# Kernel optimization log

Measured on AMD Instinct MI355X. Metric: run time of the kernel, lower is better.

## Reference

```python
import jax, jax.numpy as jnp
import numpy as np

N_HEAD = 12
CTX = 2048
FUT = 16
EPS = 1e-5


def _layer_norm(x, w, b):
    m = x.mean(-1, keepdims=True)
    v = ((x - m) ** 2).mean(-1, keepdims=True)
    return (x - m) / jnp.sqrt(v + EPS) * w + b


def setup_inputs() -> dict:
    key = jax.random.key(0)
    ks = jax.random.split(key, 10)
    C = 768
    hs = C // N_HEAD
    B, T = 1, 2048
    std = 0.02
    inp = {
        "x": jax.random.normal(ks[0], (B, T, C), jnp.float32),
        "ln1_w": jnp.ones((C,), jnp.float32),
        "ln1_b": jnp.zeros((C,), jnp.float32),
        "attn_w": jax.random.normal(ks[1], (C, 3 * C), jnp.float32) * std,
        "attn_b": jnp.zeros((3 * C,), jnp.float32),
        "fk_w": jax.random.normal(ks[2], (N_HEAD, hs, CTX - 1), jnp.float32) * std,
        "fk_b": jnp.zeros((N_HEAD, 1, CTX - 1), jnp.float32),
        "fv_w": jax.random.normal(ks[3], (N_HEAD, CTX - 1, hs), jnp.float32) * std,
        "fv_b": jnp.zeros((N_HEAD, 1, hs), jnp.float32),
        "proj_w": jax.random.normal(ks[4], (C, C), jnp.float32) * std,
        "proj_b": jnp.zeros((C,), jnp.float32),
        "ln2_w": jnp.ones((C,), jnp.float32),
        "ln2_b": jnp.zeros((C,), jnp.float32),
        "ff_w1": jax.random.normal(ks[5], (C, 4 * C), jnp.float32) * std,
        "ff_b1": jnp.zeros((4 * C,), jnp.float32),
        "ff_w2": jax.random.normal(ks[6], (4 * C, C), jnp.float32) * std,
        "ff_b2": jnp.zeros((C,), jnp.float32),
    }
    return inp


def _block(x, ln1_w, ln1_b, attn_w, attn_b, fk_w, fk_b, fv_w, fv_b,
           proj_w, proj_b, ln2_w, ln2_b, ff_w1, ff_b1, ff_w2, ff_b2):
    B, T, C = x.shape
    hs = C // N_HEAD
    T_wf = min(T + FUT, CTX)          # static
    F1 = T_wf - 1
    scale = hs ** (-0.5)

    h = _layer_norm(x, ln1_w, ln1_b)
    qkv = h @ attn_w + attn_b
    q, k, v = jnp.split(qkv, 3, axis=-1)
    q = q.reshape(B, T, N_HEAD, hs).transpose(0, 2, 1, 3)  # [B,H,T,hs]
    k = k.reshape(B, T, N_HEAD, hs).transpose(0, 2, 1, 3)
    v = v.reshape(B, T, N_HEAD, hs).transpose(0, 2, 1, 3)

    attn = jnp.einsum('bhqd,bhkd->bhqk', q, k) * scale      # [B,H,T,T]

    causal = jnp.tril(jnp.ones((T, T), bool))
    causal_attn = jnp.where(causal, attn, 0.0)
    pad = min(FUT, CTX - T)
    if pad > 0:
        causal_attn = jnp.pad(causal_attn, ((0, 0), (0, 0), (0, 0), (0, pad)))

    # future scores via per-head dynamic linear on q
    fut_bad = (jnp.tril(jnp.ones((T, F1)), -1) + jnp.triu(jnp.ones((T, F1)), FUT)) != 0
    fattn = (jnp.einsum('bhtd,hdf->bhtf', q, fk_w[:, :, :F1]) + fk_b[:, :, :F1]) * scale
    fattn = jnp.where(fut_bad, 0.0, fattn)
    fattn = jnp.pad(fattn, ((0, 0), (0, 0), (0, 0), (1, 0)))  # [B,H,T,T_wf]

    full = causal_attn + fattn
    full_ok = jnp.tril(jnp.ones((T, T_wf), bool), FUT)
    full = jnp.where(full_ok, full, -jnp.inf)
    sm = jax.nn.softmax(full, axis=-1)

    sc = jnp.where(causal, sm[..., :T], 0.0)
    sf = jnp.where(fut_bad, 0.0, sm[..., 1:T_wf])

    causal_x = jnp.einsum('bhqk,bhkd->bhqd', sc, v)
    future_x = jnp.einsum('bhtf,hfd->bhtd', sf, fv_w[:, :F1, :]) + fv_b

    new_x = (causal_x + future_x).transpose(0, 2, 1, 3).reshape(B, T, C)
    new_x = new_x @ proj_w + proj_b

    x = x + new_x
    h2 = _layer_norm(x, ln2_w, ln2_b)
    ff = jax.nn.gelu(h2 @ ff_w1 + ff_b1, approximate=False) @ ff_w2 + ff_b2
    return x + ff


def reference(x, ln1_w, ln1_b, attn_w, attn_b, fk_w, fk_b, fv_w, fv_b,
              proj_w, proj_b, ln2_w, ln2_b, ff_w1, ff_b1, ff_w2, ff_b2):
    return _block(x, ln1_w, ln1_b, attn_w, attn_b, fk_w, fk_b, fv_w, fv_b,
                  proj_w, proj_b, ln2_w, ln2_b, ff_w1, ff_b1, ff_w2, ff_b2)
```

## Files before the change

kernel.cpp:

```cpp
#include <hip/hip_runtime.h>
#include <math.h>
#include <stdint.h>
#include <stddef.h>

typedef __bf16 bf16_t;
typedef __bf16 bf16x8 __attribute__((ext_vector_type(8)));
typedef __bf16 bf16x4 __attribute__((ext_vector_type(4)));
typedef float f32x4 __attribute__((ext_vector_type(4)));

#define DEV __device__ __forceinline__


DEV void gload_lds16(const void* g, void* l) {
  __builtin_amdgcn_global_load_lds((__attribute__((address_space(1))) void*)g,
                                   (__attribute__((address_space(3))) void*)l,
                                   16, 0, 0);
}

template <bool MAXOP>
DEV float blockReduce256(float v, float* sm) {
  const int lane = threadIdx.x & 63, wid = threadIdx.x >> 6;
#pragma unroll
  for (int o = 32; o > 0; o >>= 1) {
    float ov = __shfl_down(v, o);
    v = MAXOP ? fmaxf(v, ov) : (v + ov);
  }
  if (lane == 0) sm[wid] = v;
  __syncthreads();
  float r = MAXOP ? fmaxf(fmaxf(sm[0], sm[1]), fmaxf(sm[2], sm[3]))
                  : (sm[0] + sm[1] + sm[2] + sm[3]);
  __syncthreads();
  return r;
}

__global__ __launch_bounds__(256) void prep_kernel(
    const float* __restrict__ x, const float* __restrict__ ln1_w,
    const float* __restrict__ ln1_b, bf16_t* __restrict__ hbuf,
    const float* __restrict__ attn_w, bf16_t* __restrict__ attn_wT,
    const float* __restrict__ proj_w, bf16_t* __restrict__ proj_wT,
    const float* __restrict__ ff_w1, bf16_t* __restrict__ ff_w1T,
    const float* __restrict__ ff_w2, bf16_t* __restrict__ ff_w2T,
    const float* __restrict__ fk_w, bf16_t* __restrict__ fkT,
    const float* __restrict__ fv_w, bf16_t* __restrict__ fvT) {
  __shared__ float red[4];
  __shared__ float tile[32][33];
  const int tid = threadIdx.x;
  int bid = blockIdx.x;

  if (bid < 2048) {
    const float* row = x + (size_t)bid * 768;
    float v[3];
    float s = 0.f;
#pragma unroll
    for (int i = 0; i < 3; ++i) {
      v[i] = row[tid + i * 256];
      s += v[i];
    }
    s = blockReduce256<false>(s, red);
    const float mean = s * (1.f / 768.f);
    float s2 = 0.f;
#pragma unroll
    for (int i = 0; i < 3; ++i) {
      float d = v[i] - mean;
      s2 += d * d;
    }
    s2 = blockReduce256<false>(s2, red);
    const float rstd = rsqrtf(s2 * (1.f / 768.f) + 1e-5f);
#pragma unroll
    for (int i = 0; i < 3; ++i) {
      int c = tid + i * 256;
      hbuf[(size_t)bid * 768 + c] = (bf16_t)((v[i] - mean) * rstd * ln1_w[c] + ln1_b[c]);
    }
    return;
  }
  bid -= 2048;

  const float* in;
  bf16_t* outp;
  int ldin, ldout, R, C, bx, by;
  if (bid < 1728) {
    in = attn_w; outp = attn_wT; ldin = 2304; ldout = 768; R = 768; C = 2304;
    bx = bid % 72; by = bid / 72;
  } else if (bid < 2304) {
    int k = bid - 1728;
    in = proj_w; outp = proj_wT; ldin = 768; ldout = 768; R = 768; C = 768;
    bx = k % 24; by = k / 24;
  } else if (bid < 4608) {
    int k = bid - 2304;
    in = ff_w1; outp = ff_w1T; ldin = 3072; ldout = 768; R = 768; C = 3072;
    bx = k % 96; by = k / 96;
  } else if (bid < 6912) {
    int k = bid - 4608;
    in = ff_w2; outp = ff_w2T; ldin = 768; ldout = 3072; R = 3072; C = 768;
    bx = k % 24; by = k / 24;
  } else if (bid < 8448) {
    int k = bid - 6912;
    int z = k >> 7, r = k & 127;
    in = fk_w + (size_t)z * 64 * 2047; outp = fkT + (size_t)z * 2047 * 64;
    ldin = 2047; ldout = 64; R = 64; C = 2047;
    bx = r % 64; by = r / 64;
  } else {
    int k = bid - 8448;
    int z = k >> 7, r = k & 127;
    in = fv_w + (size_t)z * 2047 * 64; outp = fvT + (size_t)z * 64 * 2048;
    ldin = 64; ldout = 2048; R = 2047; C = 64;
    bx = r % 2; by = r / 2;
  }

  const int tx = tid & 31, ty = tid >> 5;
  const int c0 = bx * 32, r0 = by * 32;
#pragma unroll
  for (int i = 0; i < 4; ++i) {
    int r = r0 + ty + i * 8, c = c0 + tx;
    if (r < R && c < C) tile[ty + i * 8][tx] = in[(size_t)r * ldin + c];
  }
  __syncthreads();
#pragma unroll
  for (int i = 0; i < 4; ++i) {
    int orow = c0 + ty + i * 8, oc = r0 + tx;
    if (orow < C && oc < R) outp[(size_t)orow * ldout + oc] = (bf16_t)tile[tx][ty + i * 8];
  }
}

__global__ __launch_bounds__(256) void reduce_ln_kernel(
    const float* __restrict__ P, int KS, const float* __restrict__ x,
    const float* __restrict__ pb, float* __restrict__ x2,
    bf16_t* __restrict__ h2, const float* __restrict__ w,
    const float* __restrict__ b) {
  __shared__ float red[4];
  const int t = blockIdx.x, tid = threadIdx.x;
  float v[3];
  float s = 0.f;
#pragma unroll
  for (int i = 0; i < 3; ++i) {
    const int c = tid + i * 256;
    const size_t idx = (size_t)t * 768 + c;
    float a = x[idx] + pb[c];
    for (int ss = 0; ss < KS; ++ss) a += P[(size_t)ss * 2048 * 768 + idx];
    v[i] = a;
    x2[idx] = a;
    s += a;
  }
  s = blockReduce256<false>(s, red);
  const float mean = s * (1.f / 768.f);
  float s2 = 0.f;
#pragma unroll
  for (int i = 0; i < 3; ++i) {
    float d = v[i] - mean;
    s2 += d * d;
  }
  s2 = blockReduce256<false>(s2, red);
  const float rstd = rsqrtf(s2 * (1.f / 768.f) + 1e-5f);
#pragma unroll
  for (int i = 0; i < 3; ++i) {
    int c = tid + i * 256;
    h2[(size_t)t * 768 + c] = (bf16_t)((v[i] - mean) * rstd * w[c] + b[c]);
  }
}

__global__ __launch_bounds__(256) void reduce_out_kernel(
    const float* __restrict__ P, int KS, const float* __restrict__ x2,
    const float* __restrict__ bb, float* __restrict__ out) {
  const int t = blockIdx.x, tid = threadIdx.x;
#pragma unroll
  for (int i = 0; i < 3; ++i) {
    const int c = tid + i * 256;
    const size_t idx = (size_t)t * 768 + c;
    float a = x2[idx] + bb[c];
    for (int ss = 0; ss < KS; ++ss) a += P[(size_t)ss * 2048 * 768 + idx];
    out[idx] = a;
  }
}

template <int WM, int WN, int EPIL, bool OBF16, bool VT>
__global__ __launch_bounds__(256) void gemm_bt_kernel(
    const bf16_t* __restrict__ A, long long sAz, int lda,
    const bf16_t* __restrict__ Bt, long long sBz, int ldb,
    void* __restrict__ Cv, long long sCz, int ldc,
    const float* __restrict__ bias,
    const float* __restrict__ resid, long long sRz,
    bf16_t* __restrict__ vt,
    float alpha, int M, int N, int K) {
  constexpr int BM = WM * 64, BN = WN * 64;
  const int tid = threadIdx.x;
  const int lane = tid & 63, wid = tid >> 6;
  const int wr = wid / WN, wc = wid % WN;
  const int m0 = blockIdx.y * BM, n0 = blockIdx.x * BN;
  A += (long long)blockIdx.z * sAz;
  Bt += (long long)blockIdx.z * sBz;

  __shared__ alignas(16) bf16_t sA[2][BM * 64];
  __shared__ alignas(16) bf16_t sB[2][BN * 64];

  f32x4 acc[4][4] = {};

  auto stage = [&](int buf, int k0) {
#pragma unroll
    for (int it = 0; it < (BM * 8) / 256; ++it) {
      int c = it * 256 + tid;
      int row = c >> 3, slot = c & 7;
      int ss = slot ^ (row & 7);
      gload_lds16(A + (size_t)(m0 + row) * (size_t)lda + k0 + ss * 8,
                  &sA[buf][c * 8]);
    }
#pragma unroll
    for (int it = 0; it < (BN * 8) / 256; ++it) {
      int c = it * 256 + tid;
      int row = c >> 3, slot = c & 7;
      int ss = slot ^ (row & 7);
      gload_lds16(Bt + (size_t)(n0 + row) * (size_t)ldb + k0 + ss * 8,
                  &sB[buf][c * 8]);
    }
  };

  const int nk = K >> 6;
  stage(0, 0);
  __syncthreads();
  for (int ki = 0; ki < nk; ++ki) {
    if (ki + 1 < nk) stage((ki + 1) & 1, (ki + 1) << 6);
    const bf16_t* cA = sA[ki & 1];
    const bf16_t* cB = sB[ki & 1];
#pragma unroll
    for (int kk = 0; kk < 2; ++kk) {
      const int s = kk * 4 + (lane >> 4);
      bf16x8 af[4], bfr[4];
#pragma unroll
      for (int i = 0; i < 4; ++i) {
        const int arow = wr * 64 + i * 16 + (lane & 15);
        af[i] = *(const bf16x8*)&cA[arow * 64 + ((s ^ (arow & 7)) * 8)];
        const int brow = wc * 64 + i * 16 + (lane & 15);
        bfr[i] = *(const bf16x8*)&cB[brow * 64 + ((s ^ (brow & 7)) * 8)];
      }
#pragma unroll
      for (int mi = 0; mi < 4; ++mi)
#pragma unroll
        for (int ni = 0; ni < 4; ++ni)
          acc[mi][ni] = __builtin_amdgcn_mfma_f32_16x16x32_bf16(af[mi], bfr[ni], acc[mi][ni], 0, 0, 0);
    }
    __syncthreads();
  }

  float* Cf = (float*)Cv;
  bf16_t* Cb = (bf16_t*)Cv;
  const long long zc = (long long)blockIdx.z * sCz;
#pragma unroll
  for (int mi = 0; mi < 4; ++mi) {
    const int rbase = m0 + wr * 64 + mi * 16 + ((lane >> 4) * 4);
#pragma unroll
    for (int ni = 0; ni < 4; ++ni) {
      const int col = n0 + wc * 64 + ni * 16 + (lane & 15);
      const float bv = bias ? bias[col] : 0.f;
      bf16x4 vloc;
#pragma unroll
      for (int r = 0; r < 4; ++r) {
        const int row = rbase + r;
        float v = acc[mi][ni][r] * alpha + bv;
        if (EPIL == 1) v = 0.5f * v * (1.f + erff(v * 0.70710678118654752f));
        if (resid) v += resid[(long long)blockIdx.z * sRz + (size_t)row * ldc + col];
        const size_t idx = (size_t)(zc + (long long)row * ldc + col);
        if (OBF16) {
          const bf16_t bvv = (bf16_t)v;
          Cb[idx] = bvv;
          if (VT) vloc[r] = bvv;
        } else {
          Cf[idx] = v;
        }
      }
      if (VT && col >= 1536)
        *(bf16x4*)&vt[(size_t)(col - 1536) * 2048 + rbase] = vloc;
    }
  }
}

#define FLASH_TPW 8
#define FLASH_NSLOT 5
#define FLASH_BANDPART 4
__global__ __launch_bounds__(256) void flash_kernel(
    const bf16_t* __restrict__ qkv, const bf16_t* __restrict__ vT,
    const bf16_t* __restrict__ fkT, const bf16_t* __restrict__ fvT,
    const float* __restrict__ fk_b, float* __restrict__ Ouc,
    float* __restrict__ lsum) {
  const int qt = 31 - (int)blockIdx.x, h = blockIdx.y, part = blockIdx.z;
  const int ntiles = qt + 1;
  const int q0 = qt << 6;
  const int tid = threadIdx.x, lane = tid & 63, w = tid >> 6;
  __shared__ alignas(16) bf16_t sK[2][64 * 64];
  __shared__ alignas(16) bf16_t sV[2][64 * 64];
  __shared__ alignas(16) bf16_t sP[4][16 * 128];

  const int l15 = lane & 15, l4 = lane >> 4;
  const int rloc = w * 16 + (l4 << 2);
  const int rowC0 = q0 + rloc;
  bf16_t* sPw = sP[w];

  if (part != FLASH_BANDPART) {
    const int kt0 = part * FLASH_TPW;
    if (kt0 >= ntiles) return;
  }

  const int qrow = q0 + w * 16 + l15;
  bf16x8 aq[2];
#pragma unroll
  for (int kk = 0; kk < 2; ++kk)
    aq[kk] = *(const bf16x8*)&qkv[(size_t)qrow * 2304 + h * 64 + 8 * l4 + 32 * kk];

  f32x4 o[4] = {};
  float lacc[4] = {0.f, 0.f, 0.f, 0.f};

  if (part == FLASH_BANDPART) {
    const int t0 = q0;
    bf16_t* sKb = &sK[0][0];
    bf16_t* sVb = &sV[0][0];
#pragma unroll
    for (int it = 0; it < 3; ++it) {
      const int c = it * 256 + tid;
      if (c < 640) {
        const int row = c >> 3, slot = c & 7;
        const int ss = slot ^ (row & 7);
        const int srow = min(t0 + row, 2046);
        gload_lds16(fkT + ((size_t)h * 2047 + srow) * 64 + ss * 8, &sKb[c * 8]);
      }
    }
#pragma unroll
    for (int it = 0; it < 4; ++it) {
      const int c = it * 256 + tid;
      const int row = c >> 4, slot = c & 15;
      const int ss = slot ^ (row & 7);
      gload_lds16(fvT + ((size_t)h * 64 + row) * 2048 + t0 + ss * 8, &sVb[c * 8]);
    }
    __syncthreads();

    f32x4 s[6] = {};
    __builtin_amdgcn_s_setprio(1);
#pragma unroll
    for (int kk = 0; kk < 2; ++kk)
#pragma unroll
      for (int ni = 0; ni < 5; ++ni) {
        const int row = ni * 16 + l15;
        const int slot = l4 + 4 * kk;
        bf16x8 bfk = *(const bf16x8*)&sKb[row * 64 + ((slot ^ (row & 7)) * 8)];
        s[ni] = __builtin_amdgcn_mfma_f32_16x16x32_bf16(aq[kk], bfk, s[ni], 0, 0, 0);
      }
    __builtin_amdgcn_s_setprio(0);
    float fkb_v[5];
#pragma unroll
    for (int ni = 0; ni < 5; ++ni)
      fkb_v[ni] = fk_b[h * 2047 + min(t0 + ni * 16 + l15, 2046)];

#pragma unroll
    for (int ni = 0; ni < 6; ++ni) {
      const int c = ni * 16 + l15;
      const int colb = c * 2;
#pragma unroll
      for (int r = 0; r < 4; ++r) {
        const int j = c - (rloc + r);
        const bool ok = (ni < 5) && (j >= 0) && (j < 16) && (t0 + c < 2047);
        const float pv = ok ? __expf((s[ni][r] + fkb_v[ni < 5 ? ni : 0]) * 0.125f) : 0.f;
        lacc[r] += pv;
        const int pr = (l4 << 2) + r;
        *(bf16_t*)((char*)sPw + ((pr * 256 + colb) ^ ((pr & 7) << 4))) = (bf16_t)pv;
      }
    }

    __builtin_amdgcn_s_setprio(1);
#pragma unroll
    for (int kk = 0; kk < 3; ++kk) {
      const int slot = l4 + 4 * kk;
      bf16x8 ap = *(const bf16x8*)((char*)sPw + (l15 * 256 + ((slot ^ (l15 & 7)) * 16)));
#pragma unroll
      for (int ni = 0; ni < 4; ++ni) {
        const int vrow = ni * 16 + l15;
        bf16x8 bv = *(const bf16x8*)&sVb[vrow * 128 + ((slot ^ (vrow & 7)) * 8)];
        o[ni] = __builtin_amdgcn_mfma_f32_16x16x32_bf16(ap, bv, o[ni], 0, 0, 0);
      }
    }
    __builtin_amdgcn_s_setprio(0);
  } else {
    const int kt0 = part * FLASH_TPW;
    const int kt1 = min(kt0 + FLASH_TPW, ntiles);

    auto stage = [&](int buf, int kt) {
      const int t0 = kt << 6;
#pragma unroll
      for (int it = 0; it < 2; ++it) {
        const int c = it * 256 + tid;
        const int row = c >> 3, slot = c & 7;
        const int ss = slot ^ (row & 7);
        gload_lds16(qkv + (size_t)(t0 + row) * 2304 + 768 + h * 64 + ss * 8,
                    &sK[buf][c * 8]);
        gload_lds16(vT + ((size_t)h * 64 + row) * 2048 + t0 + ss * 8,
                    &sV[buf][c * 8]);
      }
    };

    stage(0, kt0);
    __syncthreads();

    for (int kt = kt0; kt < kt1; ++kt) {
      const int buf = (kt - kt0) & 1;
      if (kt + 1 < kt1) stage(buf ^ 1, kt + 1);
      const int t0 = kt << 6;

      f32x4 s[4] = {};
      __builtin_amdgcn_s_setprio(1);
#pragma unroll
      for (int kk = 0; kk < 2; ++kk)
#pragma unroll
        for (int ni = 0; ni < 4; ++ni) {
          const int row = ni * 16 + l15;
          const int slot = l4 + 4 * kk;
          bf16x8 bfk = *(const bf16x8*)&sK[buf][row * 64 + ((slot ^ (row & 7)) * 8)];
          s[ni] = __builtin_amdgcn_mfma_f32_16x16x32_bf16(aq[kk], bfk, s[ni], 0, 0, 0);
        }
      __builtin_amdgcn_s_setprio(0);

      const bool full = (t0 + 63 <= q0);
#pragma unroll
      for (int ni = 0; ni < 4; ++ni) {
        const int col = t0 + ni * 16 + l15;
        const int colb = (ni * 16 + l15) * 2;
#pragma unroll
        for (int r = 0; r < 4; ++r) {
          const bool ok = full || (col <= rowC0 + r);
          const float pv = ok ? __expf(s[ni][r] * 0.125f) : 0.f;
          lacc[r] += pv;
          const int pr = (l4 << 2) + r;
          *(bf16_t*)((char*)sPw + ((pr * 256 + colb) ^ ((pr & 7) << 4))) = (bf16_t)pv;
        }
      }

      __builtin_amdgcn_s_setprio(1);
#pragma unroll
      for (int kk = 0; kk < 2; ++kk) {
        const int slot = l4 + 4 * kk;
        bf16x8 ap = *(const bf16x8*)((char*)sPw + (l15 * 256 + ((slot ^ (l15 & 7)) * 16)));
#pragma unroll
        for (int ni = 0; ni < 4; ++ni) {
          const int vrow = ni * 16 + l15;
          bf16x8 bv = *(const bf16x8*)&sV[buf][vrow * 64 + ((slot ^ (vrow & 7)) * 8)];
          o[ni] = __builtin_amdgcn_mfma_f32_16x16x32_bf16(ap, bv, o[ni], 0, 0, 0);
        }
      }
      __builtin_amdgcn_s_setprio(0);
      __syncthreads();
    }
  }

  float* Oh = Ouc + (((size_t)h * 32 + qt) * FLASH_NSLOT + part) * 4096;
#pragma unroll
  for (int ni = 0; ni < 4; ++ni) {
    const int col = ni * 16 + l15;
#pragma unroll
    for (int r = 0; r < 4; ++r) Oh[(size_t)(rloc + r) * 64 + col] = o[ni][r];
  }
#pragma unroll
  for (int off = 1; off < 16; off <<= 1)
#pragma unroll
    for (int r = 0; r < 4; ++r) lacc[r] += __shfl_xor(lacc[r], off);
  if (l15 == 0) {
#pragma unroll
    for (int r = 0; r < 4; ++r)
      lsum[((size_t)h * 2048 + rowC0 + r) * FLASH_NSLOT + part] = lacc[r];
  }
}

__global__ __launch_bounds__(256) void combine_kernel(
    const float* __restrict__ Ouc, const float* __restrict__ lsum,
    const float* __restrict__ fv_b, bf16_t* __restrict__ attn_o) {
  const int t = blockIdx.x * 4 + (threadIdx.x >> 6);
  const int h = blockIdx.y, lane = threadIdx.x & 63;
  const int qt = t >> 6;
  const int nparts = (qt + FLASH_TPW) / FLASH_TPW;
  const float* Ob = Ouc + ((size_t)h * 32 + qt) * FLASH_NSLOT * 4096 +
                    (t & 63) * 64 + lane;
  const float* lb = lsum + ((size_t)h * 2048 + t) * FLASH_NSLOT;
  float l_run = lb[FLASH_BANDPART];
  float O_run = Ob[(size_t)FLASH_BANDPART * 4096];
  for (int p = 0; p < nparts; ++p) {
    l_run += lb[p];
    O_run += Ob[(size_t)p * 4096];
  }
  const float val = O_run / l_run + fv_b[h * 64 + lane];
  attn_o[(size_t)t * 768 + h * 64 + lane] = (bf16_t)val;
}


extern "C" void kernel_launch(void* const* d_in, const int* in_sizes, int n_in,
                              void* d_out, int out_size, void* d_ws, size_t ws_size,
                              hipStream_t stream) {
  (void)in_sizes; (void)n_in; (void)out_size;
  const float* x      = (const float*)d_in[0];
  const float* ln1_w  = (const float*)d_in[1];
  const float* ln1_b  = (const float*)d_in[2];
  const float* attn_w = (const float*)d_in[3];
  const float* attn_b = (const float*)d_in[4];
  const float* fk_w   = (const float*)d_in[5];
  const float* fk_b   = (const float*)d_in[6];
  const float* fv_w   = (const float*)d_in[7];
  const float* fv_b   = (const float*)d_in[8];
  const float* proj_w = (const float*)d_in[9];
  const float* proj_b = (const float*)d_in[10];
  const float* ln2_w  = (const float*)d_in[11];
  const float* ln2_b  = (const float*)d_in[12];
  const float* ff_w1  = (const float*)d_in[13];
  const float* ff_b1  = (const float*)d_in[14];
  const float* ff_w2  = (const float*)d_in[15];
  const float* ff_b2  = (const float*)d_in[16];
  float* out = (float*)d_out;

  char* wsp = (char*)d_ws;
  size_t off = 0;
  auto alloc = [&](size_t bytes) -> void* {
    void* r = wsp + off;
    off += (bytes + 255) & ~(size_t)255;
    return r;
  };

  bf16_t* hbuf    = (bf16_t*)alloc((size_t)2048 * 768 * 2);
  bf16_t* attn_wT = (bf16_t*)alloc((size_t)2304 * 768 * 2);
  bf16_t* proj_wT = (bf16_t*)alloc((size_t)768 * 768 * 2);
  bf16_t* ff_w1T  = (bf16_t*)alloc((size_t)3072 * 768 * 2);
  bf16_t* ff_w2T  = (bf16_t*)alloc((size_t)768 * 3072 * 2);
  bf16_t* fkT     = (bf16_t*)alloc((size_t)12 * 2047 * 64 * 2);
  bf16_t* fvT     = (bf16_t*)alloc(((size_t)12 * 64 * 2048 + 512) * 2);
  bf16_t* qkv     = (bf16_t*)alloc((size_t)2048 * 2304 * 2);
  bf16_t* vT      = (bf16_t*)alloc((size_t)12 * 64 * 2048 * 2);
  bf16_t* attn_o  = (bf16_t*)alloc((size_t)2048 * 768 * 2);
  float*  x2      = (float*)alloc((size_t)2048 * 768 * 4);
  bf16_t* h2      = (bf16_t*)alloc((size_t)2048 * 768 * 2);
  bf16_t* gbuf    = (bf16_t*)alloc((size_t)2048 * 3072 * 2);
  float*  Ouc     = (float*)alloc((size_t)12 * 32 * FLASH_NSLOT * 4096 * 4);
  float*  lsb     = (float*)alloc((size_t)12 * 2048 * FLASH_NSLOT * 4);

  const size_t slice = (size_t)2048 * 768 * 4;
  long long remain = ((long long)ws_size - (long long)off) / (long long)slice;
  int KS2 = 6;
  while (KS2 > 1 && ((3072 / KS2) % 64 != 0 || (3072 % KS2) != 0 || KS2 > remain)) --KS2;
  int KS1 = 4;
  while (KS1 > 1 && ((768 / KS1) % 64 != 0 || (768 % KS1) != 0 || KS1 > remain)) --KS1;
  int KSmax = KS1 > KS2 ? KS1 : KS2;
  float* Ppart = (float*)alloc((size_t)KSmax * slice);

  prep_kernel<<<12032, 256, 0, stream>>>(x, ln1_w, ln1_b, hbuf,
                                         attn_w, attn_wT, proj_w, proj_wT,
                                         ff_w1, ff_w1T, ff_w2, ff_w2T,
                                         fk_w, fkT, fv_w, fvT);

  gemm_bt_kernel<2, 2, 0, true, true><<<dim3(18, 16, 1), 256, 0, stream>>>(
      hbuf, 0, 768, attn_wT, 0, 768, qkv, 0, 2304, attn_b, nullptr, 0, vT,
      1.f, 2048, 2304, 768);

  flash_kernel<<<dim3(32, 12, FLASH_NSLOT), 256, 0, stream>>>(
      qkv, vT, fkT, fvT, fk_b, Ouc, lsb);

  combine_kernel<<<dim3(512, 12), 256, 0, stream>>>(Ouc, lsb, fv_b, attn_o);

  {
    const int KC = 768 / KS1;
    gemm_bt_kernel<2, 2, 0, false, false><<<dim3(6, 16, KS1), 256, 0, stream>>>(
        attn_o, KC, 768, proj_wT, KC, 768, Ppart, 2048LL * 768, 768, nullptr,
        nullptr, 0, nullptr, 1.f, 2048, 768, KC);
  }
  reduce_ln_kernel<<<2048, 256, 0, stream>>>(Ppart, KS1, x, proj_b, x2, h2,
                                             ln2_w, ln2_b);

  gemm_bt_kernel<2, 2, 1, true, false><<<dim3(24, 16, 1), 256, 0, stream>>>(
      h2, 0, 768, ff_w1T, 0, 768, gbuf, 0, 3072, ff_b1, nullptr, 0, nullptr,
      1.f, 2048, 3072, 768);

  {
    const int KC = 3072 / KS2;
    gemm_bt_kernel<2, 2, 0, false, false><<<dim3(6, 16, KS2), 256, 0, stream>>>(
        gbuf, KC, 3072, ff_w2T, KC, 3072, Ppart, 2048LL * 768, 768, nullptr,
        nullptr, 0, nullptr, 1.f, 2048, 768, KC);
  }
  reduce_out_kernel<<<2048, 256, 0, stream>>>(Ppart, KS2, x2, ff_b2, out);
}
```

Before: 154.9 us.

## Overlap GEMM tile prefetch via partial vmcnt waits; fold attention band into causal part

In the bf16 GEMM, the full __syncthreads after each k-step becomes an explicit s_waitcnt vmcnt(8) plus barrier. The next stage's global-to-LDS loads can now stay in flight while the current tile is consumed, instead of being drained every iteration. In the flash attention kernel, the separate future-band partition is removed and its work is appended to whichever causal partition holds the diagonal tile. This cuts the slot count from 5 to 4, removes extra blocks, and lightens the combine pass. The cost is a longer serial path for the block that now also does the band work, and a hardcoded vmcnt value that assumes exactly 8 loads per stage.

After: 164.4 us. 1.06x slower.

```diff
diff --git a/kernel.cpp b/kernel.cpp
--- a/kernel.cpp
+++ b/kernel.cpp
@@ -181,6 +181,7 @@
     const float* __restrict__ resid, long long sRz,
     bf16_t* __restrict__ vt,
     float alpha, int M, int N, int K) {
+  static_assert(WM == 2 && WN == 2, "vmcnt(8) assumes 8 loads/stage");
   constexpr int BM = WM * 64, BN = WN * 64;
   const int tid = threadIdx.x;
   const int lane = tid & 63, wid = tid >> 6;
@@ -215,11 +216,21 @@
 
   const int nk = K >> 6;
   stage(0, 0);
-  __syncthreads();
+  asm volatile("s_waitcnt vmcnt(0)" ::: "memory");
+  __builtin_amdgcn_s_barrier();
+  __builtin_amdgcn_sched_barrier(0);
   for (int ki = 0; ki < nk; ++ki) {
-    if (ki + 1 < nk) stage((ki + 1) & 1, (ki + 1) << 6);
-    const bf16_t* cA = sA[ki & 1];
-    const bf16_t* cB = sB[ki & 1];
+    const int buf = ki & 1;
+    if (ki + 1 < nk) {
+      stage(buf ^ 1, (ki + 1) << 6);
+      asm volatile("s_waitcnt vmcnt(8)" ::: "memory");
+    } else {
+      asm volatile("s_waitcnt vmcnt(0)" ::: "memory");
+    }
+    __builtin_amdgcn_s_barrier();
+    __builtin_amdgcn_sched_barrier(0);
+    const bf16_t* cA = sA[buf];
+    const bf16_t* cB = sB[buf];
 #pragma unroll
     for (int kk = 0; kk < 2; ++kk) {
       const int s = kk * 4 + (lane >> 4);
@@ -237,7 +248,9 @@
         for (int ni = 0; ni < 4; ++ni)
           acc[mi][ni] = __builtin_amdgcn_mfma_f32_16x16x32_bf16(af[mi], bfr[ni], acc[mi][ni], 0, 0, 0);
     }
-    __syncthreads();
+    __builtin_amdgcn_sched_barrier(0);
+    __builtin_amdgcn_s_barrier();
+    __builtin_amdgcn_sched_barrier(0);
   }
 
   float* Cf = (float*)Cv;
@@ -273,8 +286,7 @@
 }
 
 #define FLASH_TPW 8
-#define FLASH_NSLOT 5
-#define FLASH_BANDPART 4
+#define FLASH_NSLOT 4
 __global__ __launch_bounds__(256) void flash_kernel(
     const bf16_t* __restrict__ qkv, const bf16_t* __restrict__ vT,
     const bf16_t* __restrict__ fkT, const bf16_t* __restrict__ fvT,
@@ -283,6 +295,10 @@
   const int qt = 31 - (int)blockIdx.x, h = blockIdx.y, part = blockIdx.z;
   const int ntiles = qt + 1;
   const int q0 = qt << 6;
+  const int kt0 = part * FLASH_TPW;
+  if (kt0 >= ntiles) return;
+  const int kt1 = min(kt0 + FLASH_TPW, ntiles);
+  const bool has_band = (part == (qt >> 3));
   const int tid = threadIdx.x, lane = tid & 63, w = tid >> 6;
   __shared__ alignas(16) bf16_t sK[2][64 * 64];
   __shared__ alignas(16) bf16_t sV[2][64 * 64];
@@ -293,11 +309,6 @@
   const int rowC0 = q0 + rloc;
   bf16_t* sPw = sP[w];
 
-  if (part != FLASH_BANDPART) {
-    const int kt0 = part * FLASH_TPW;
-    if (kt0 >= ntiles) return;
-  }
-
   const int qrow = q0 + w * 16 + l15;
   bf16x8 aq[2];
 #pragma unroll
@@ -307,7 +318,73 @@
   f32x4 o[4] = {};
   float lacc[4] = {0.f, 0.f, 0.f, 0.f};
 
-  if (part == FLASH_BANDPART) {
+  auto stage = [&](int buf, int kt) {
+    const int t0 = kt << 6;
+#pragma unroll
+    for (int it = 0; it < 2; ++it) {
+      const int c = it * 256 + tid;
+      const int row = c >> 3, slot = c & 7;
+      const int ss = slot ^ (row & 7);
+      gload_lds16(qkv + (size_t)(t0 + row) * 2304 + 768 + h * 64 + ss * 8,
+                  &sK[buf][c * 8]);
+      gload_lds16(vT + ((size_t)h * 64 + row) * 2048 + t0 + ss * 8,
+                  &sV[buf][c * 8]);
+    }
+  };
+
+  stage(0, kt0);
+  __syncthreads();
+
+  for (int kt = kt0; kt < kt1; ++kt) {
+    const int buf = (kt - kt0) & 1;
+    if (kt + 1 < kt1) stage(buf ^ 1, kt + 1);
+    const int t0 = kt << 6;
+
+    f32x4 s[4] = {};
+    __builtin_amdgcn_s_setprio(1);
+#pragma unroll
+    for (int kk = 0; kk < 2; ++kk)
+#pragma unroll
+      for (int ni = 0; ni < 4; ++ni) {
+        const int row = ni * 16 + l15;
+        const int slot = l4 + 4 * kk;
+        bf16x8 bfk = *(const bf16x8*)&sK[buf][row * 64 + ((slot ^ (row & 7)) * 8)];
+        s[ni] = __builtin_amdgcn_mfma_f32_16x16x32_bf16(aq[kk], bfk, s[ni], 0, 0, 0);
+      }
+    __builtin_amdgcn_s_setprio(0);
+
+    const bool full = (t0 + 63 <= q0);
+#pragma unroll
+    for (int ni = 0; ni < 4; ++ni) {
+      const int col = t0 + ni * 16 + l15;
+      const int colb = (ni * 16 + l15) * 2;
+#pragma unroll
+      for (int r = 0; r < 4; ++r) {
+        const bool ok = full || (col <= rowC0 + r);
+        const float pv = ok ? __expf(s[ni][r] * 0.125f) : 0.f;
+        lacc[r] += pv;
+        const int pr = (l4 << 2) + r;
+        *(bf16_t*)((char*)sPw + ((pr * 256 + colb) ^ ((pr & 7) << 4))) = (bf16_t)pv;
+      }
+    }
+
+    __builtin_amdgcn_s_setprio(1);
+#pragma unroll
+    for (int kk = 0; kk < 2; ++kk) {
+      const int slot = l4 + 4 * kk;
+      bf16x8 ap = *(const bf16x8*)((char*)sPw + (l15 * 256 + ((slot ^ (l15 & 7)) * 16)));
+#pragma unroll
+      for (int ni = 0; ni < 4; ++ni) {
+        const int vrow = ni * 16 + l15;
+        bf16x8 bv = *(const bf16x8*)&sV[buf][vrow * 64 + ((slot ^ (vrow & 7)) * 8)];
+        o[ni] = __builtin_amdgcn_mfma_f32_16x16x32_bf16(ap, bv, o[ni], 0, 0, 0);
+      }
+    }
+    __builtin_amdgcn_s_setprio(0);
+    __syncthreads();
+  }
+
+  if (has_band) {
     const int t0 = q0;
     bf16_t* sKb = &sK[0][0];
     bf16_t* sVb = &sV[0][0];
@@ -375,75 +452,6 @@
       }
     }
     __builtin_amdgcn_s_setprio(0);
-  } else {
-    const int kt0 = part * FLASH_TPW;
-    const int kt1 = min(kt0 + FLASH_TPW, ntiles);
-
-    auto stage = [&](int buf, int kt) {
-      const int t0 = kt << 6;
-#pragma unroll
-      for (int it = 0; it < 2; ++it) {
-        const int c = it * 256 + tid;
-        const int row = c >> 3, slot = c & 7;
-        const int ss = slot ^ (row & 7);
-        gload_lds16(qkv + (size_t)(t0 + row) * 2304 + 768 + h * 64 + ss * 8,
-                    &sK[buf][c * 8]);
-        gload_lds16(vT + ((size_t)h * 64 + row) * 2048 + t0 + ss * 8,
-                    &sV[buf][c * 8]);
-      }
-    };
-
-    stage(0, kt0);
-    __syncthreads();
-
-    for (int kt = kt0; kt < kt1; ++kt) {
-      const int buf = (kt - kt0) & 1;
-      if (kt + 1 < kt1) stage(buf ^ 1, kt + 1);
-      const int t0 = kt << 6;
-
-      f32x4 s[4] = {};
-      __builtin_amdgcn_s_setprio(1);
-#pragma unroll
-      for (int kk = 0; kk < 2; ++kk)
-#pragma unroll
-        for (int ni = 0; ni < 4; ++ni) {
-          const int row = ni * 16 + l15;
-          const int slot = l4 + 4 * kk;
-          bf16x8 bfk = *(const bf16x8*)&sK[buf][row * 64 + ((slot ^ (row & 7)) * 8)];
-          s[ni] = __builtin_amdgcn_mfma_f32_16x16x32_bf16(aq[kk], bfk, s[ni], 0, 0, 0);
-        }
-      __builtin_amdgcn_s_setprio(0);
-
-      const bool full = (t0 + 63 <= q0);
-#pragma unroll
-      for (int ni = 0; ni < 4; ++ni) {
-        const int col = t0 + ni * 16 + l15;
-        const int colb = (ni * 16 + l15) * 2;
-#pragma unroll
-        for (int r = 0; r < 4; ++r) {
-          const bool ok = full || (col <= rowC0 + r);
-          const float pv = ok ? __expf(s[ni][r] * 0.125f) : 0.f;
-          lacc[r] += pv;
-          const int pr = (l4 << 2) + r;
-          *(bf16_t*)((char*)sPw + ((pr * 256 + colb) ^ ((pr & 7) << 4))) = (bf16_t)pv;
-        }
-      }
-
-      __builtin_amdgcn_s_setprio(1);
-#pragma unroll
-      for (int kk = 0; kk < 2; ++kk) {
-        const int slot = l4 + 4 * kk;
-        bf16x8 ap = *(const bf16x8*)((char*)sPw + (l15 * 256 + ((slot ^ (l15 & 7)) * 16)));
-#pragma unroll
-        for (int ni = 0; ni < 4; ++ni) {
-          const int vrow = ni * 16 + l15;
-          bf16x8 bv = *(const bf16x8*)&sV[buf][vrow * 64 + ((slot ^ (vrow & 7)) * 8)];
-          o[ni] = __builtin_amdgcn_mfma_f32_16x16x32_bf16(ap, bv, o[ni], 0, 0, 0);
-        }
-      }
-      __builtin_amdgcn_s_setprio(0);
-      __syncthreads();
-    }
   }
 
   float* Oh = Ouc + (((size_t)h * 32 + qt) * FLASH_NSLOT + part) * 4096;
@@ -474,8 +482,7 @@
   const float* Ob = Ouc + ((size_t)h * 32 + qt) * FLASH_NSLOT * 4096 +
                     (t & 63) * 64 + lane;
   const float* lb = lsum + ((size_t)h * 2048 + t) * FLASH_NSLOT;
-  float l_run = lb[FLASH_BANDPART];
-  float O_run = Ob[(size_t)FLASH_BANDPART * 4096];
+  float l_run = 0.f, O_run = 0.f;
   for (int p = 0; p < nparts; ++p) {
     l_run += lb[p];
     O_run += Ob[(size_t)p * 4096];
```
